# Performance work log

Hardware: AMD Instinct MI355X
Metric: run time of the kernel (lower is better)

Reference implementation:

```python
import jax, jax.numpy as jnp
import numpy as np
import math

B, N, T, F_IN, F_OUT = 8, 512, 12, 32, 64


def setup_inputs() -> dict:
    key = jax.random.key(0)
    k1, k2, k3, k4, k5 = jax.random.split(key, 5)
    x = jax.random.normal(k1, (B, N, T, F_IN), dtype=jnp.float32)
    phaseAct_matrix = jax.random.uniform(k2, (B, T, N, N), dtype=jnp.float32)
    adj = jax.random.uniform(k3, (N, N), dtype=jnp.float32)  # sym-normalized adjacency stand-in
    mask = (jax.random.uniform(k4, (N,)) < 0.5).astype(jnp.float32)  # 1 = observed node, 0 = unknown
    theta = jax.random.normal(k5, (F_IN, F_OUT), dtype=jnp.float32) * 0.05
    return {"x": x, "phaseAct_matrix": phaseAct_matrix, "adj": adj, "mask": mask, "theta": theta}


def _spatial_attention(x):
    # x: (B, N, T, F) -> scores (B, T, N, N)
    f = x.shape[-1]
    xt = x.transpose(0, 2, 1, 3)  # (B, T, N, F)
    score = jnp.einsum('btnf,btmf->btnm', xt, xt) / math.sqrt(f)
    return jax.nn.softmax(score, axis=-1)


def reference(x, phaseAct_matrix, adj, mask, theta):
    f = x.shape[-1]
    t_steps = x.shape[2]
    inv_sqrt_f = 1.0 / math.sqrt(f)
    m = mask[None, :, None, None]  # broadcast over (B, N, T-1, F)

    def body(i, x_cur):
        sa = _spatial_attention(x_cur) * inv_sqrt_f          # (B, T, N, N)
        sat_act = (phaseAct_matrix * sa).transpose(0, 1, 3, 2)  # (B, T, N, N) transposed
        xt = x_cur.transpose(0, 2, 1, 3)                     # (B, T, N, F)
        # predict step t from step t-1: (B, T-1, N, F)
        x_pred = jnp.einsum('btnm,btmf->btnf', sat_act[:, 1:], xt[:, :t_steps - 1])
        x_pred = x_pred.transpose(0, 2, 1, 3)                # (B, N, T-1, F)
        # revise_unknown: keep observed nodes, impute unknown nodes at steps 1..T-1
        x_rev = x_cur[:, :, 1:, :] * m + x_pred * (1.0 - m)
        return jnp.concatenate([x_cur[:, :, 0:1, :], x_rev], axis=2)

    x = jax.lax.fori_loop(1, t_steps, body, x)

    sa = _spatial_attention(x) * inv_sqrt_f                  # (B, T, N, N)
    satAct_adj = phaseAct_matrix * adj[None, None] * sa      # (B, T, N, N)
    xt = x.transpose(0, 2, 1, 3)                             # (B, T, N, F)
    agg = jnp.einsum('btmn,btmf->btnf', satAct_adj, xt)      # transpose(adj) @ x
    out = jax.nn.relu(jnp.einsum('btnf,fo->btno', agg, theta))  # (B, T, N, F_out)
    return out.transpose(0, 2, 1, 3)                         # (B, N, T, F_out)
```

## Files before the change

### kernel.cpp

```cpp
#include <hip/hip_runtime.h>


#define B_ 8
#define N_ 512
#define T_ 12
#define F_ 32
#define O_ 64

typedef unsigned int uint_t;
typedef unsigned short ushort_t;
typedef _Float16 f16_t;
typedef _Float16 f16x4 __attribute__((ext_vector_type(4)));
typedef _Float16 f16x8 __attribute__((ext_vector_type(8)));
typedef float f32x4 __attribute__((ext_vector_type(4)));

__device__ __forceinline__ int xidx(int b, int n, int t, int f) {
    return ((b * N_ + n) * T_ + t) * F_ + f;
}
__device__ __forceinline__ f16x8 load_frag8(const float* p) {
    float4 a = *reinterpret_cast<const float4*>(p);
    float4 b = *reinterpret_cast<const float4*>(p + 4);
    f16x8 r;
    r[0] = (f16_t)a.x; r[1] = (f16_t)a.y; r[2] = (f16_t)a.z; r[3] = (f16_t)a.w;
    r[4] = (f16_t)b.x; r[5] = (f16_t)b.y; r[6] = (f16_t)b.z; r[7] = (f16_t)b.w;
    return r;
}
union U2H4 { uint2 u; f16x4 h; };

__global__ __launch_bounds__(256)
void permute_kernel(const float* __restrict__ src, ushort_t* __restrict__ dst)
{
    __shared__ float Lp[16][516];
    const int tid = threadIdx.x;
    const int mc  = blockIdx.x;
    const int s   = blockIdx.y;
    src += (size_t)s * N_ * N_ + (size_t)mc * 16 * N_;
    uint_t* dstu = (uint_t*)dst + (size_t)s * 131072 + (size_t)mc * 4096;

    #pragma unroll
    for (int k = 0; k < 32; ++k) {
        int idx = tid + 256 * k;
        Lp[idx >> 9][idx & 511] = src[idx];
    }
    __syncthreads();
    #pragma unroll
    for (int k = 0; k < 16; ++k) {
        int u    = tid + 256 * k;
        int nt   = u >> 7;
        int r    = u & 127;
        int quad = r >> 5;
        int cl   = (r >> 1) & 15;
        int m0   = quad * 4 + (r & 1) * 2;
        int n    = nt * 16 + cl;
        union { f16_t h[2]; uint_t i; } pk;
        pk.h[0] = (f16_t)Lp[m0][n];
        pk.h[1] = (f16_t)Lp[m0 + 1][n];
        dstu[u] = pk.i;
    }
}

template <int FINAL>
__global__ __launch_bounds__(256)
void stats_kernel(const float* __restrict__ x0,
                  const float* __restrict__ xcur,
                  float2* __restrict__ MS)
{
    const int tid  = threadIdx.x;
    const int w    = tid >> 6;
    const int l    = tid & 63;
    const int quad = l >> 4;
    const int col  = l & 15;
    const int t    = FINAL ? blockIdx.y : blockIdx.y + 1;
    const int b    = blockIdx.z;
    const int mb   = (blockIdx.x * 4 + w) * 16;
    const float inv_f = 0.17677669529663687f;
    const float* xs = (FINAL && t == 0) ? x0 : xcur;

    f16x8 bm = load_frag8(&xs[xidx(b, mb + col, t, quad * 8)]);

    float M = -1e30f, S = 0.f;
    #pragma unroll 4
    for (int nt = 0; nt < 32; ++nt) {
        f16x8 an = load_frag8(&xs[xidx(b, nt * 16 + col, t, quad * 8)]);
        f32x4 s4 = __builtin_amdgcn_mfma_f32_16x16x32_f16(
                       an, bm, (f32x4){0.f, 0.f, 0.f, 0.f}, 0, 0, 0);
        float m4 = fmaxf(fmaxf(s4[0], s4[1]), fmaxf(s4[2], s4[3])) * inv_f;
        float Mn = fmaxf(M, m4);
        S = S * __expf(M - Mn)
          + (__expf(s4[0] * inv_f - Mn) + __expf(s4[1] * inv_f - Mn))
          + (__expf(s4[2] * inv_f - Mn) + __expf(s4[3] * inv_f - Mn));
        M = Mn;
    }
    #pragma unroll
    for (int d = 16; d < 64; d <<= 1) {
        float Mo = __shfl_xor(M, d, 64), So = __shfl_xor(S, d, 64);
        float Mn = fmaxf(M, Mo);
        S = S * __expf(M - Mn) + So * __expf(Mo - Mn);
        M = Mn;
    }
    if (l < 16)
        MS[(size_t)(b * T_ + t) * N_ + mb + l] = make_float2(M, inv_f / S);
}

template <int FINAL>
__global__ __launch_bounds__(256)
void pred_kernel(const float* __restrict__ x0,
                 const float* __restrict__ xcur,
                 float* __restrict__ dst,
                 const ushort_t* __restrict__ phase_h,
                 const ushort_t* __restrict__ adj_h,
                 const float* __restrict__ mask,
                 const float2* __restrict__ MS)
{
    const int tid  = threadIdx.x;
    const int w    = tid >> 6;
    const int l    = tid & 63;
    const int quad = l >> 4;
    const int col  = l & 15;
    const int t    = FINAL ? blockIdx.y : blockIdx.y + 1;
    const int b    = blockIdx.z;
    const int nt   = blockIdx.x * 4 + w;
    const float inv_f = 0.17677669529663687f;

    const float* xs     = (FINAL && t == 0) ? x0 : xcur;
    const float* xp_src = FINAL ? xs : ((t == 1) ? x0 : xcur);
    const int    tp     = FINAL ? t : t - 1;

    f16x8 bf = load_frag8(&xs[xidx(b, nt * 16 + col, t, quad * 8)]);
    const uint_t* phu = (const uint_t*)phase_h + (size_t)(b * T_ + t) * 131072
                        + nt * 128 + l * 2;
    const uint_t* adu = (const uint_t*)adj_h + nt * 128 + l * 2;
    const float2* msp = MS + (size_t)(b * T_ + t) * N_ + quad * 4;

    f32x4 acc0 = (f32x4){0.f, 0.f, 0.f, 0.f};
    f32x4 acc1 = (f32x4){0.f, 0.f, 0.f, 0.f};

    #pragma unroll 2
    for (int c = 0; c < 32; ++c) {
        const int mb = c * 16;
        f16x8 af = load_frag8(&xs[xidx(b, mb + col, t, quad * 8)]);
        U2H4 ph; ph.u = *(const uint2*)(phu + (size_t)c * 4096);
        U2H4 aj;
        if (FINAL) aj.u = *(const uint2*)(adu + (size_t)c * 4096);
        float4 msA = *(const float4*)(msp + mb);
        float4 msB = *(const float4*)(msp + mb + 2);
        f16x4 bp0, bp1;
        #pragma unroll
        for (int j = 0; j < 4; ++j) {
            bp0[j] = (f16_t)xp_src[xidx(b, mb + quad * 4 + j, tp, col)];
            bp1[j] = (f16_t)xp_src[xidx(b, mb + quad * 4 + j, tp, 16 + col)];
        }

        f32x4 s4 = __builtin_amdgcn_mfma_f32_16x16x32_f16(
                       af, bf, (f32x4){0.f, 0.f, 0.f, 0.f}, 0, 0, 0);

        const float Mv[4] = {msA.x, msA.z, msB.x, msB.z};
        const float Sv[4] = {msA.y, msA.w, msB.y, msB.w};
        f16x4 wf;
        #pragma unroll
        for (int v = 0; v < 4; ++v) {
            float e = __expf(s4[v] * inv_f - Mv[v]) * Sv[v] * (float)ph.h[v];
            if (FINAL) e *= (float)aj.h[v];
            wf[v] = (f16_t)e;
        }
        acc0 = __builtin_amdgcn_mfma_f32_16x16x16f16(wf, bp0, acc0, 0, 0, 0);
        acc1 = __builtin_amdgcn_mfma_f32_16x16x16f16(wf, bp1, acc1, 0, 0, 0);
    }

    #pragma unroll
    for (int v = 0; v < 4; ++v) {
        const int n = nt * 16 + quad * 4 + v;
        if (FINAL) {
            float* d0 = &dst[((size_t)(b * T_ + t) * N_ + n) * F_ + col];
            d0[0]  = acc0[v];
            d0[16] = acc1[v];
        } else {
            const int i0 = xidx(b, n, t, col);
            const float mk = mask[n];
            dst[i0]      = (mk != 0.f) ? xcur[i0]      : acc0[v];
            dst[i0 + 16] = (mk != 0.f) ? xcur[i0 + 16] : acc1[v];
        }
    }
}

__global__ __launch_bounds__(256)
void proj_kernel(const float* __restrict__ agg, const float* __restrict__ theta,
                 float* __restrict__ out)
{
    __shared__ float th[F_ * O_];
    int tid = threadIdx.x;
    #pragma unroll
    for (int p = 0; p < 8; ++p) th[tid + 256 * p] = theta[tid + 256 * p];
    __syncthreads();
    int g  = blockIdx.x * 256 + tid;
    int o  = g & 63;
    int r  = g >> 6;
    int tt = r % T_;
    int r2 = r / T_;
    int n  = r2 & 511;
    int b  = r2 >> 9;
    const float* a = &agg[((b * T_ + tt) * N_ + n) * F_];
    float s = 0.f;
    #pragma unroll
    for (int f = 0; f < F_; ++f) s += a[f] * th[f * O_ + o];
    out[g] = fmaxf(s, 0.f);
}

extern "C" void kernel_launch(void* const* d_in, const int* in_sizes, int n_in,
                              void* d_out, int out_size, void* d_ws, size_t ws_size,
                              hipStream_t stream)
{
    const float* x     = (const float*)d_in[0];
    const float* phase = (const float*)d_in[1];
    const float* adj   = (const float*)d_in[2];
    const float* mask  = (const float*)d_in[3];
    const float* theta = (const float*)d_in[4];
    float* out = (float*)d_out;

    const size_t XE = (size_t)B_ * N_ * T_ * F_;
    float*    xA      = (float*)d_ws;
    float*    xB      = xA + XE;
    float*    agg     = xB + XE;
    ushort_t* phase_h = (ushort_t*)(agg + XE);
    ushort_t* adj_h   = phase_h + (size_t)96 * N_ * N_;
    float2*   MS      = (float2*)(adj_h + (size_t)N_ * N_);

    permute_kernel<<<dim3(32, 96), 256, 0, stream>>>(phase, phase_h);
    permute_kernel<<<dim3(32, 1), 256, 0, stream>>>(adj, adj_h);

    const float* cur = x;
    float* bufs[2] = { xA, xB };
    for (int i = 0; i < T_ - 1; ++i) {
        float* nxt = bufs[i & 1];
        stats_kernel<0><<<dim3(8, T_ - 1, B_), 256, 0, stream>>>(x, cur, MS);
        pred_kernel<0><<<dim3(8, T_ - 1, B_), 256, 0, stream>>>(
            x, cur, nxt, phase_h, adj_h, mask, MS);
        cur = nxt;
    }
    stats_kernel<1><<<dim3(8, T_, B_), 256, 0, stream>>>(x, cur, MS);
    pred_kernel<1><<<dim3(8, T_, B_), 256, 0, stream>>>(
        x, cur, agg, phase_h, adj_h, mask, MS);
    proj_kernel<<<(B_ * N_ * T_ * O_) / 256, 256, 0, stream>>>(agg, theta, out);
}
```

Baseline: 957.6 us.

## Widen fp16 phase/adj layout to 16-byte loads and split softmax stats accumulators

Result: slower. 1.007 ms (+5.2%).

```diff
diff --git a/kernel.cpp b/kernel.cpp
--- a/kernel.cpp
+++ b/kernel.cpp
@@ -30,37 +30,39 @@
 __global__ __launch_bounds__(256)
 void permute_kernel(const float* __restrict__ src, ushort_t* __restrict__ dst)
 {
-    __shared__ float Lp[16][516];
+    __shared__ float Lp[32][516];
     const int tid = threadIdx.x;
-    const int mc  = blockIdx.x;
+    const int cp  = blockIdx.x;
     const int s   = blockIdx.y;
-    src += (size_t)s * N_ * N_ + (size_t)mc * 16 * N_;
-    uint_t* dstu = (uint_t*)dst + (size_t)s * 131072 + (size_t)mc * 4096;
-
-    #pragma unroll
-    for (int k = 0; k < 32; ++k) {
+    src += (size_t)s * N_ * N_ + (size_t)cp * 32 * N_;
+    uint4* dstu = (uint4*)dst + (size_t)s * 32768 + (size_t)cp * 2048;
+
+    #pragma unroll
+    for (int k = 0; k < 64; ++k) {
         int idx = tid + 256 * k;
         Lp[idx >> 9][idx & 511] = src[idx];
     }
     __syncthreads();
     #pragma unroll
-    for (int k = 0; k < 16; ++k) {
+    for (int k = 0; k < 8; ++k) {
         int u    = tid + 256 * k;
-        int nt   = u >> 7;
-        int r    = u & 127;
-        int quad = r >> 5;
-        int cl   = (r >> 1) & 15;
-        int m0   = quad * 4 + (r & 1) * 2;
+        int nt   = u >> 6;
+        int l    = u & 63;
+        int quad = l >> 4;
+        int cl   = l & 15;
         int n    = nt * 16 + cl;
-        union { f16_t h[2]; uint_t i; } pk;
-        pk.h[0] = (f16_t)Lp[m0][n];
-        pk.h[1] = (f16_t)Lp[m0 + 1][n];
-        dstu[u] = pk.i;
+        int r0   = quad * 4;
+        union { f16_t h[2]; uint_t i; } p0, p1, p2, p3;
+        p0.h[0] = (f16_t)Lp[r0][n];      p0.h[1] = (f16_t)Lp[r0 + 1][n];
+        p1.h[0] = (f16_t)Lp[r0 + 2][n];  p1.h[1] = (f16_t)Lp[r0 + 3][n];
+        p2.h[0] = (f16_t)Lp[16 + r0][n];     p2.h[1] = (f16_t)Lp[16 + r0 + 1][n];
+        p3.h[0] = (f16_t)Lp[16 + r0 + 2][n]; p3.h[1] = (f16_t)Lp[16 + r0 + 3][n];
+        dstu[u] = make_uint4(p0.i, p1.i, p2.i, p3.i);
     }
 }
 
 template <int FINAL>
-__global__ __launch_bounds__(256)
+__global__ __launch_bounds__(256, 4)
 void stats_kernel(const float* __restrict__ x0,
                   const float* __restrict__ xcur,
                   float2* __restrict__ MS)
@@ -78,32 +80,43 @@
 
     f16x8 bm = load_frag8(&xs[xidx(b, mb + col, t, quad * 8)]);
 
-    float M = -1e30f, S = 0.f;
-    #pragma unroll 4
-    for (int nt = 0; nt < 32; ++nt) {
-        f16x8 an = load_frag8(&xs[xidx(b, nt * 16 + col, t, quad * 8)]);
-        f32x4 s4 = __builtin_amdgcn_mfma_f32_16x16x32_f16(
-                       an, bm, (f32x4){0.f, 0.f, 0.f, 0.f}, 0, 0, 0);
-        float m4 = fmaxf(fmaxf(s4[0], s4[1]), fmaxf(s4[2], s4[3])) * inv_f;
-        float Mn = fmaxf(M, m4);
-        S = S * __expf(M - Mn)
-          + (__expf(s4[0] * inv_f - Mn) + __expf(s4[1] * inv_f - Mn))
-          + (__expf(s4[2] * inv_f - Mn) + __expf(s4[3] * inv_f - Mn));
-        M = Mn;
-    }
+    float M[4] = {-1e30f, -1e30f, -1e30f, -1e30f};
+    float S[4] = {0.f, 0.f, 0.f, 0.f};
+    #pragma unroll 2
+    for (int base = 0; base < 8; ++base) {
+        #pragma unroll
+        for (int ss = 0; ss < 4; ++ss) {
+            const int nt2 = base * 4 + ss;
+            f16x8 an = load_frag8(&xs[xidx(b, nt2 * 16 + col, t, quad * 8)]);
+            f32x4 s4 = __builtin_amdgcn_mfma_f32_16x16x32_f16(
+                           an, bm, (f32x4){0.f, 0.f, 0.f, 0.f}, 0, 0, 0);
+            float m4 = fmaxf(fmaxf(s4[0], s4[1]), fmaxf(s4[2], s4[3])) * inv_f;
+            float Mn = fmaxf(M[ss], m4);
+            S[ss] = S[ss] * __expf(M[ss] - Mn)
+                  + (__expf(s4[0] * inv_f - Mn) + __expf(s4[1] * inv_f - Mn))
+                  + (__expf(s4[2] * inv_f - Mn) + __expf(s4[3] * inv_f - Mn));
+            M[ss] = Mn;
+        }
+    }
+    float M01 = fmaxf(M[0], M[1]);
+    float S01 = S[0] * __expf(M[0] - M01) + S[1] * __expf(M[1] - M01);
+    float M23 = fmaxf(M[2], M[3]);
+    float S23 = S[2] * __expf(M[2] - M23) + S[3] * __expf(M[3] - M23);
+    float Mm  = fmaxf(M01, M23);
+    float Sm  = S01 * __expf(M01 - Mm) + S23 * __expf(M23 - Mm);
     #pragma unroll
     for (int d = 16; d < 64; d <<= 1) {
-        float Mo = __shfl_xor(M, d, 64), So = __shfl_xor(S, d, 64);
-        float Mn = fmaxf(M, Mo);
-        S = S * __expf(M - Mn) + So * __expf(Mo - Mn);
-        M = Mn;
+        float Mo = __shfl_xor(Mm, d, 64), So = __shfl_xor(Sm, d, 64);
+        float Mn = fmaxf(Mm, Mo);
+        Sm = Sm * __expf(Mm - Mn) + So * __expf(Mo - Mn);
+        Mm = Mn;
     }
     if (l < 16)
-        MS[(size_t)(b * T_ + t) * N_ + mb + l] = make_float2(M, inv_f / S);
+        MS[(size_t)(b * T_ + t) * N_ + mb + l] = make_float2(Mm, inv_f / Sm);
 }
 
 template <int FINAL>
-__global__ __launch_bounds__(256)
+__global__ __launch_bounds__(256, 3)
 void pred_kernel(const float* __restrict__ x0,
                  const float* __restrict__ xcur,
                  float* __restrict__ dst,
@@ -127,44 +140,64 @@
     const int    tp     = FINAL ? t : t - 1;
 
     f16x8 bf = load_frag8(&xs[xidx(b, nt * 16 + col, t, quad * 8)]);
-    const uint_t* phu = (const uint_t*)phase_h + (size_t)(b * T_ + t) * 131072
-                        + nt * 128 + l * 2;
-    const uint_t* adu = (const uint_t*)adj_h + nt * 128 + l * 2;
+    const uint4* phu4 = (const uint4*)phase_h + (size_t)(b * T_ + t) * 32768
+                        + nt * 64 + l;
+    const uint4* adu4 = (const uint4*)adj_h + nt * 64 + l;
     const float2* msp = MS + (size_t)(b * T_ + t) * N_ + quad * 4;
 
     f32x4 acc0 = (f32x4){0.f, 0.f, 0.f, 0.f};
     f32x4 acc1 = (f32x4){0.f, 0.f, 0.f, 0.f};
 
     #pragma unroll 2
-    for (int c = 0; c < 32; ++c) {
-        const int mb = c * 16;
-        f16x8 af = load_frag8(&xs[xidx(b, mb + col, t, quad * 8)]);
-        U2H4 ph; ph.u = *(const uint2*)(phu + (size_t)c * 4096);
-        U2H4 aj;
-        if (FINAL) aj.u = *(const uint2*)(adu + (size_t)c * 4096);
-        float4 msA = *(const float4*)(msp + mb);
-        float4 msB = *(const float4*)(msp + mb + 2);
-        f16x4 bp0, bp1;
+    for (int cp = 0; cp < 16; ++cp) {
+        const int mb0 = cp * 32;
+        const int mb1 = mb0 + 16;
+        uint4 phq = phu4[cp * 2048];
+        uint4 ajq;
+        if (FINAL) ajq = adu4[cp * 2048];
+        f16x8 af0 = load_frag8(&xs[xidx(b, mb0 + col, t, quad * 8)]);
+        f16x8 af1 = load_frag8(&xs[xidx(b, mb1 + col, t, quad * 8)]);
+        float4 msA0 = *(const float4*)(msp + mb0);
+        float4 msB0 = *(const float4*)(msp + mb0 + 2);
+        float4 msA1 = *(const float4*)(msp + mb1);
+        float4 msB1 = *(const float4*)(msp + mb1 + 2);
+        f16x4 bp00, bp01, bp10, bp11;
         #pragma unroll
-        for (int j = 0; j < 4; ++j) {
-            bp0[j] = (f16_t)xp_src[xidx(b, mb + quad * 4 + j, tp, col)];
-            bp1[j] = (f16_t)xp_src[xidx(b, mb + quad * 4 + j, tp, 16 + col)];
-        }
-
-        f32x4 s4 = __builtin_amdgcn_mfma_f32_16x16x32_f16(
-                       af, bf, (f32x4){0.f, 0.f, 0.f, 0.f}, 0, 0, 0);
-
-        const float Mv[4] = {msA.x, msA.z, msB.x, msB.z};
-        const float Sv[4] = {msA.y, msA.w, msB.y, msB.w};
-        f16x4 wf;
+        for (int jj = 0; jj < 4; ++jj) {
+            bp00[jj] = (f16_t)xp_src[xidx(b, mb0 + quad * 4 + jj, tp, col)];
+            bp01[jj] = (f16_t)xp_src[xidx(b, mb0 + quad * 4 + jj, tp, 16 + col)];
+            bp10[jj] = (f16_t)xp_src[xidx(b, mb1 + quad * 4 + jj, tp, col)];
+            bp11[jj] = (f16_t)xp_src[xidx(b, mb1 + quad * 4 + jj, tp, 16 + col)];
+        }
+
+        f32x4 s40 = __builtin_amdgcn_mfma_f32_16x16x32_f16(
+                        af0, bf, (f32x4){0.f, 0.f, 0.f, 0.f}, 0, 0, 0);
+        f32x4 s41 = __builtin_amdgcn_mfma_f32_16x16x32_f16(
+                        af1, bf, (f32x4){0.f, 0.f, 0.f, 0.f}, 0, 0, 0);
+
+        U2H4 p0; p0.u = make_uint2(phq.x, phq.y);
+        U2H4 p1; p1.u = make_uint2(phq.z, phq.w);
+        U2H4 a0, a1;
+        if (FINAL) { a0.u = make_uint2(ajq.x, ajq.y); a1.u = make_uint2(ajq.z, ajq.w); }
+
+        const float Mv0[4] = {msA0.x, msA0.z, msB0.x, msB0.z};
+        const float Sv0[4] = {msA0.y, msA0.w, msB0.y, msB0.w};
+        const float Mv1[4] = {msA1.x, msA1.z, msB1.x, msB1.z};
+        const float Sv1[4] = {msA1.y, msA1.w, msB1.y, msB1.w};
+
+        f16x4 wf0, wf1;
         #pragma unroll
         for (int v = 0; v < 4; ++v) {
-            float e = __expf(s4[v] * inv_f - Mv[v]) * Sv[v] * (float)ph.h[v];
-            if (FINAL) e *= (float)aj.h[v];
-            wf[v] = (f16_t)e;
-        }
-        acc0 = __builtin_amdgcn_mfma_f32_16x16x16f16(wf, bp0, acc0, 0, 0, 0);
-        acc1 = __builtin_amdgcn_mfma_f32_16x16x16f16(wf, bp1, acc1, 0, 0, 0);
+            float e0 = __expf(s40[v] * inv_f - Mv0[v]) * Sv0[v] * (float)p0.h[v];
+            float e1 = __expf(s41[v] * inv_f - Mv1[v]) * Sv1[v] * (float)p1.h[v];
+            if (FINAL) { e0 *= (float)a0.h[v]; e1 *= (float)a1.h[v]; }
+            wf0[v] = (f16_t)e0;
+            wf1[v] = (f16_t)e1;
+        }
+        acc0 = __builtin_amdgcn_mfma_f32_16x16x16f16(wf0, bp00, acc0, 0, 0, 0);
+        acc1 = __builtin_amdgcn_mfma_f32_16x16x16f16(wf0, bp01, acc1, 0, 0, 0);
+        acc0 = __builtin_amdgcn_mfma_f32_16x16x16f16(wf1, bp10, acc0, 0, 0, 0);
+        acc1 = __builtin_amdgcn_mfma_f32_16x16x16f16(wf1, bp11, acc1, 0, 0, 0);
     }
 
     #pragma unroll
@@ -225,8 +258,8 @@
     ushort_t* adj_h   = phase_h + (size_t)96 * N_ * N_;
     float2*   MS      = (float2*)(adj_h + (size_t)N_ * N_);
 
-    permute_kernel<<<dim3(32, 96), 256, 0, stream>>>(phase, phase_h);
-    permute_kernel<<<dim3(32, 1), 256, 0, stream>>>(adj, adj_h);
+    permute_kernel<<<dim3(16, 96), 256, 0, stream>>>(phase, phase_h);
+    permute_kernel<<<dim3(16, 1), 256, 0, stream>>>(adj, adj_h);
 
     const float* cur = x;
     float* bufs[2] = { xA, xB };
```
